# Performance work log

Measured on AMD Instinct MI355X. Metric: run time of the kernel, lower is better.

The kernel has to match this reference:

```python
import jax, jax.numpy as jnp
import numpy as np

# dims
N_USER = 30000; N_ITEM = 30000; HID = 256; HEADS = 4; DH = HID // HEADS
L = 2; E_BUYS = 200000
IMG_D = 512; TASTE_D = 768; NUTR_D = 20; LR = 64; IMG_RANK = 64
EPS = 1e-5
# node type order: 0=user 1=item 2=taste 3=intention 4=image
# edge type order: taste->item, intention->item, image->item, user->item (buys), item->user (bought_by)


def _bn(x, g, b):
    # nn.BatchNorm1d in training mode (biased variance), deterministic
    mu = jnp.mean(x, axis=0)
    var = jnp.mean((x - mu) ** 2, axis=0)
    return (x - mu) * jax.lax.rsqrt(var + EPS) * g + b


def _segment_softmax(logits, seg, n):
    m = jax.ops.segment_max(logits, seg, num_segments=n)
    m = jnp.where(jnp.isfinite(m), m, 0.0)
    e = jnp.exp(logits - m[seg])
    s = jax.ops.segment_sum(e, seg, num_segments=n)
    return e / (s[seg] + 1e-16)


def _model(p, user_id, item_id, buys_src, buys_dst):
    # --- encoders (dropout = identity in eval) ---
    xu = jax.nn.relu(_bn(p['user_emb'][user_id] @ p['user_W'] + p['user_b'], p['user_bn_g'], p['user_bn_b']))
    xi = jax.nn.relu(_bn(p['item_emb'][item_id] @ p['item_W'] + p['item_b'], p['item_bn_g'], p['item_bn_b']))
    ximg = (p['image_feat'] @ p['img_U']) @ p['img_V'] + p['img_b']  # LowRankLinear
    xt = p['taste_feat'] @ p['taste_W'] + p['taste_b']
    xn = p['intent_feat'] @ p['intent_W'] + p['intent_b']
    xs = [xu, xi, xt, xn, ximg]
    assoc = jnp.arange(N_ITEM, dtype=jnp.int32)
    # (src_type, dst_type, src_idx, dst_idx)
    edges = [(2, 1, assoc, assoc), (3, 1, assoc, assoc), (4, 1, assoc, assoc),
             (0, 1, buys_src, buys_dst), (1, 0, buys_dst, buys_src)]
    scale = 1.0 / np.sqrt(DH)
    n_of = [N_USER, N_ITEM]
    for l in range(L):
        k, q, v = [], [], []
        for t in range(5):
            kqv = xs[t] @ p['kqv_W'][l, t] + p['kqv_b'][l, t]
            kk, qq, vv = jnp.split(kqv, 3, axis=1)
            k.append(kk.reshape(-1, HEADS, DH))
            q.append(qq.reshape(-1, HEADS, DH))
            v.append(vv.reshape(-1, HEADS, DH))
        buf = {0: [], 1: []}
        for e, (s, d, si, di) in enumerate(edges):
            # relation-specific per-head transforms of source k/v (all src nodes, then gather)
            ke = jnp.einsum('nhd,hde->nhe', k[s], p['k_rel'][l, e])
            ve = jnp.einsum('nhd,hde->nhe', v[s], p['v_rel'][l, e])
            logit = jnp.sum(q[d][di] * ke[si], axis=-1) * p['p_rel'][l, e] * scale  # [E,H]
            buf[d].append((logit, ve[si], di))
        new_xs = list(xs)
        for d in (0, 1):  # dst node types: user, item
            logits = jnp.concatenate([b[0] for b in buf[d]], axis=0)
            msgs = jnp.concatenate([b[1] for b in buf[d]], axis=0)
            dsts = jnp.concatenate([b[2] for b in buf[d]], axis=0)
            alpha = _segment_softmax(logits, dsts, n_of[d])  # softmax over ALL incoming edges per dst node
            agg = jax.ops.segment_sum(alpha[:, :, None] * msgs, dsts, num_segments=n_of[d])
            o = jax.nn.gelu(agg.reshape(-1, HID), approximate=False) @ p['out_W'][l, d] + p['out_b'][l, d]
            sg = jax.nn.sigmoid(p['skip'][l, d])
            o = sg * o + (1.0 - sg) * xs[d]  # HGTConv learned skip
            o = o + xs[d]                    # MultiModalFusionGAT residual
            o = jax.nn.relu(_bn(o, p['fbn_g'][l, d], p['fbn_b'][l, d]))  # per-type BN+ReLU (dropout eval)
            new_xs[d] = o
        xs = new_xs  # taste/intention/image pass through unchanged
    return jnp.stack(xs, axis=0)  # [5, 30000, HID]


def setup_inputs():
    key = jax.random.key(0)
    ks = iter(jax.random.split(key, 48))
    def nrm(shape, scale=0.05):
        return jax.random.normal(next(ks), shape, dtype=jnp.float32) * scale
    z = lambda *s: jnp.zeros(s, jnp.float32)
    o = lambda *s: jnp.ones(s, jnp.float32)
    inp = {}
    inp['user_id'] = jnp.arange(N_USER, dtype=jnp.int32)
    inp['item_id'] = jnp.arange(N_ITEM, dtype=jnp.int32)
    inp['buys_src'] = jax.random.randint(next(ks), (E_BUYS,), 0, N_USER, dtype=jnp.int32)
    inp['buys_dst'] = jax.random.randint(next(ks), (E_BUYS,), 0, N_ITEM, dtype=jnp.int32)
    inp['image_feat'] = nrm((N_ITEM, IMG_D), 1.0)
    inp['taste_feat'] = nrm((N_ITEM, TASTE_D), 1.0)
    inp['intent_feat'] = nrm((N_ITEM, NUTR_D), 1.0)
    inp['user_emb'] = nrm((N_USER, LR), 0.1)
    inp['user_W'] = nrm((LR, HID)); inp['user_b'] = z(HID)
    inp['user_bn_g'] = o(HID); inp['user_bn_b'] = z(HID)
    inp['item_emb'] = nrm((N_ITEM, LR), 0.1)
    inp['item_W'] = nrm((LR, HID)); inp['item_b'] = z(HID)
    inp['item_bn_g'] = o(HID); inp['item_bn_b'] = z(HID)
    inp['img_U'] = nrm((IMG_D, IMG_RANK)); inp['img_V'] = nrm((IMG_RANK, HID)); inp['img_b'] = z(HID)
    inp['taste_W'] = nrm((TASTE_D, HID)); inp['taste_b'] = z(HID)
    inp['intent_W'] = nrm((NUTR_D, HID)); inp['intent_b'] = z(HID)
    inp['kqv_W'] = nrm((L, 5, HID, 3 * HID)); inp['kqv_b'] = z(L, 5, 3 * HID)
    inp['out_W'] = nrm((L, 5, HID, HID)); inp['out_b'] = z(L, 5, HID)
    inp['k_rel'] = nrm((L, 5, HEADS, DH, DH))
    inp['v_rel'] = nrm((L, 5, HEADS, DH, DH))
    inp['p_rel'] = o(L, 5, HEADS)
    inp['skip'] = o(L, 5)
    inp['fbn_g'] = o(L, 2, HID); inp['fbn_b'] = z(L, 2, HID)
    return inp


def reference(user_id, item_id, buys_src, buys_dst, image_feat, taste_feat, intent_feat,
              user_emb, user_W, user_b, user_bn_g, user_bn_b,
              item_emb, item_W, item_b, item_bn_g, item_bn_b,
              img_U, img_V, img_b, taste_W, taste_b, intent_W, intent_b,
              kqv_W, kqv_b, out_W, out_b, k_rel, v_rel, p_rel, skip, fbn_g, fbn_b):
    p = dict(image_feat=image_feat, taste_feat=taste_feat, intent_feat=intent_feat,
             user_emb=user_emb, user_W=user_W, user_b=user_b, user_bn_g=user_bn_g, user_bn_b=user_bn_b,
             item_emb=item_emb, item_W=item_W, item_b=item_b, item_bn_g=item_bn_g, item_bn_b=item_bn_b,
             img_U=img_U, img_V=img_V, img_b=img_b, taste_W=taste_W, taste_b=taste_b,
             intent_W=intent_W, intent_b=intent_b, kqv_W=kqv_W, kqv_b=kqv_b, out_W=out_W, out_b=out_b,
             k_rel=k_rel, v_rel=v_rel, p_rel=p_rel, skip=skip, fbn_g=fbn_g, fbn_b=fbn_b)
    return _model(p, user_id, item_id, buys_src, buys_dst)
```

## Files before the change

### kernel.cpp

```cpp
#include <hip/hip_runtime.h>
#include <math.h>

#define HID 256
#define EBUY 200000
#define NNODE 30000
#define MP 30080
static const size_t S  = (size_t)NNODE * HID;
static const size_t SP = (size_t)MP * HID;

typedef __attribute__((ext_vector_type(8))) short  short8;
typedef __attribute__((ext_vector_type(4))) float  f32x4;

#define OFF_TASTE 0
#define OFF_INT   196608
#define OFF_IMGU  204800
#define OFF_IMGV  237568
#define OFF_USER  253952
#define OFF_ITEM  270336
#define OFF_OUTW  286720
#define WENC_TOT  548864

__device__ __forceinline__ float gelu_f(float x) {
    return 0.5f * x * (1.0f + erff(x * 0.70710678118654752f));
}
__device__ __forceinline__ unsigned short f2bf(float f) {
    unsigned u = __float_as_uint(f);
    u = (u + 0x7FFFu + ((u >> 16) & 1u)) >> 16;
    return (unsigned short)u;
}
__device__ __forceinline__ float b2f(unsigned short us) {
    return __uint_as_float((unsigned)us << 16);
}
__device__ __forceinline__ void gl_lds16(const unsigned short* g, unsigned short* l) {
    __builtin_amdgcn_global_load_lds(
        (const __attribute__((address_space(1))) unsigned int*)g,
        (__attribute__((address_space(3))) unsigned int*)l, 16, 0, 0);
}

__global__ void conv_pad(const float* __restrict__ in, unsigned short* __restrict__ o,
                         int M, int K, int Kpad)
{
    int i = blockIdx.x * 256 + threadIdx.x;
    if (i >= M * Kpad) return;
    int r = i / Kpad, k = i % Kpad;
    o[i] = (k < K) ? f2bf(in[(size_t)r * K + k]) : (unsigned short)0;
}

__global__ void wtconv_all(const float* __restrict__ taste_W, const float* __restrict__ intent_W,
                           const float* __restrict__ img_U, const float* __restrict__ img_V,
                           const float* __restrict__ user_W, const float* __restrict__ item_W,
                           const float* __restrict__ out_W, unsigned short* __restrict__ WENC)
{
    int i = blockIdx.x * 256 + threadIdx.x;
    if (i >= WENC_TOT) return;
    const float* W; int K, N, Kpad, idx;
    if (i < OFF_INT)        { W = taste_W;  K = 768; N = 256; Kpad = 768; idx = i - OFF_TASTE; }
    else if (i < OFF_IMGU)  { W = intent_W; K = 20;  N = 256; Kpad = 32;  idx = i - OFF_INT; }
    else if (i < OFF_IMGV)  { W = img_U;    K = 512; N = 64;  Kpad = 512; idx = i - OFF_IMGU; }
    else if (i < OFF_USER)  { W = img_V;    K = 64;  N = 256; Kpad = 64;  idx = i - OFF_IMGV; }
    else if (i < OFF_ITEM)  { W = user_W;   K = 64;  N = 256; Kpad = 64;  idx = i - OFF_USER; }
    else if (i < OFF_OUTW)  { W = item_W;   K = 64;  N = 256; Kpad = 64;  idx = i - OFF_ITEM; }
    else {
        int k = (i - OFF_OUTW) >> 16;
        int l = k >> 1, d = k & 1;
        W = out_W + (size_t)(l * 5 + d) * 65536;
        K = 256; N = 256; Kpad = 256; idx = (i - OFF_OUTW) & 65535;
    }
    int n = idx / Kpad, kk = idx % Kpad;
    WENC[i] = (kk < K) ? f2bf(W[(size_t)kk * N + n]) : (unsigned short)0;
}

__global__ void build_kqv(const float* __restrict__ kqv_W, const float* __restrict__ kqv_b,
                          const float* __restrict__ k_rel, const float* __restrict__ v_rel,
                          unsigned short* __restrict__ WKV, float* __restrict__ bKV,
                          unsigned short* __restrict__ WQ, float* __restrict__ bQ)
{
    int s = blockIdx.y;
    int l = s / 5, t = s % 5;
    static const int es[5] = {3, 4, 0, 1, 2};
    int e = es[t];
    int tid = blockIdx.x * 256 + threadIdx.x;
    if (tid >= 257 * 768) return;
    int r = tid / 768, c = tid % 768;
    int cb = c >> 8, cc = c & 255;
    int h = cc >> 6, dd = cc & 63;
    const float* W = kqv_W + (size_t)s * 196608;
    const float* bv = kqv_b + (size_t)s * 768;
    const float* Wrow = (r < 256) ? (W + (size_t)r * 768) : bv;
    if (cb == 1) {
        if (t >= 2) return;
        float outv = Wrow[256 + cc];
        if (r < 256) WQ[(size_t)(l * 2 + t) * 65536 + (size_t)cc * 256 + r] = f2bf(outv);
        else         bQ[(l * 2 + t) * 256 + cc] = outv;
        return;
    }
    const float* R = ((cb == 0) ? k_rel : v_rel) + (size_t)(l * 5 + e) * 16384 + (size_t)h * 4096;
    int sb = (cb == 0) ? 0 : 512;
    float sum = 0.f;
    #pragma unroll 8
    for (int d = 0; d < 64; ++d)
        sum += Wrow[sb + h * 64 + d] * R[d * 64 + dd];
    int col = (cb == 0) ? cc : 256 + cc;
    if (r < 256) WKV[(size_t)s * 131072 + (size_t)col * 256 + r] = f2bf(sum);
    else         bKV[s * 512 + col] = sum;
}

template<int AF32, int GATH2, int BSEL, int EPI>
__launch_bounds__(256)
__global__ void gemm_mfma(const void* __restrict__ Ap, const void* __restrict__ Ap2,
                          const int* __restrict__ g1, const int* __restrict__ g2,
                          const unsigned short* __restrict__ BT0, int bStride,
                          const float* __restrict__ bias0, const float* __restrict__ bias1,
                          int biasStride,
                          float* __restrict__ D0, unsigned short* __restrict__ Db,
                          unsigned short* __restrict__ Db2,
                          int M, int N, int K,
                          const float* __restrict__ skipP, const float* __restrict__ resid,
                          float* __restrict__ bns)
{
    __shared__ union {
        unsigned short AB[4][4096];
        unsigned short O[16384];
    } sm;
    const int tid = threadIdx.x;
    const int gx = gridDim.x;
    int bid = blockIdx.y * gx + blockIdx.x;
    {
        int nwg = gx * gridDim.y;
        int q = nwg >> 3, r = nwg & 7;
        int xc = bid & 7, i = bid >> 3;
        int base = (xc < r) ? xc * (q + 1) : r * (q + 1) + (xc - r) * q;
        bid = base + i;
    }
    const int bx = bid % gx, by = bid / gx;
    const int row0 = by * 128, col0 = bx * 128;
    const int wid = tid >> 6, lane = tid & 63;
    const int wr = wid >> 1, wc = wid & 1;
    const int l16 = lane & 15, kg = lane >> 4;
    const int tt = (BSEL || GATH2) ? (by / 235) : 0;

    const unsigned short* BT = BT0 + (size_t)tt * bStride;
    const float* bias = bias0;
    if (GATH2)              bias = tt ? bias1 : bias0;
    else if (BSEL && bias0) bias = bias0 + (size_t)tt * biasStride;

    f32x4 acc[4][4];
    const f32x4 zero = {0.f, 0.f, 0.f, 0.f};
    #pragma unroll
    for (int i = 0; i < 4; ++i)
        #pragma unroll
        for (int j = 0; j < 4; ++j) acc[i][j] = zero;

    const int lrow = lane >> 2, lchk = lane & 3;
    int cB0 = min(col0 + wid * 32 + lrow, N - 1);
    int cB1 = min(col0 + wid * 32 + 16 + lrow, N - 1);
    const unsigned short* Bp0 = BT + (size_t)cB0 * K + lchk * 8;
    const unsigned short* Bp1 = BT + (size_t)cB1 * K + lchk * 8;
    const int ofs0 = wid * 1024;
    const int ofs1 = wid * 1024 + 512;

    const unsigned short* Ap0b = nullptr; const unsigned short* Ap1b = nullptr;
    const float* Af0 = nullptr; const float* Af1 = nullptr;
    const int rA0 = tid >> 2, rA1 = (tid >> 2) + 64;
    const int q0 = tid & 3;
    if (GATH2) {
        int lr0 = row0 + rA0 - tt * MP; if (lr0 >= NNODE) lr0 = NNODE - 1;
        int lr1 = row0 + rA1 - tt * MP; if (lr1 >= NNODE) lr1 = NNODE - 1;
        const int* gA = tt ? g2 : g1;
        const float* Abase = tt ? (const float*)Ap2 : (const float*)Ap;
        Af0 = Abase + (size_t)gA[lr0] * K;
        Af1 = Abase + (size_t)gA[lr1] * K;
    } else if (AF32) {
        Af0 = (const float*)Ap + (size_t)min(row0 + rA0, M - 1) * K;
        Af1 = (const float*)Ap + (size_t)min(row0 + rA1, M - 1) * K;
    } else {
        int rr0 = min(row0 + wid * 32 + lrow, M - 1);
        int rr1 = min(row0 + wid * 32 + 16 + lrow, M - 1);
        Ap0b = (const unsigned short*)Ap + (size_t)rr0 * K + lchk * 8;
        Ap1b = (const unsigned short*)Ap + (size_t)rr1 * K + lchk * 8;
    }

    const int nt = K >> 5;
    int cur = 0;

    #define STAGE_F32(c, k0) do { \
        float4 x0 = *(const float4*)&Af0[(k0) + q0 * 8]; \
        float4 x1 = *(const float4*)&Af0[(k0) + q0 * 8 + 4]; \
        float4 y0 = *(const float4*)&Af1[(k0) + q0 * 8]; \
        float4 y1 = *(const float4*)&Af1[(k0) + q0 * 8 + 4]; \
        ushort4 u0 = {f2bf(x0.x), f2bf(x0.y), f2bf(x0.z), f2bf(x0.w)}; \
        ushort4 u1 = {f2bf(x1.x), f2bf(x1.y), f2bf(x1.z), f2bf(x1.w)}; \
        ushort4 w0 = {f2bf(y0.x), f2bf(y0.y), f2bf(y0.z), f2bf(y0.w)}; \
        ushort4 w1 = {f2bf(y1.x), f2bf(y1.y), f2bf(y1.z), f2bf(y1.w)}; \
        *(ushort4*)&sm.AB[c][rA0 * 32 + q0 * 8]     = u0; \
        *(ushort4*)&sm.AB[c][rA0 * 32 + q0 * 8 + 4] = u1; \
        *(ushort4*)&sm.AB[c][rA1 * 32 + q0 * 8]     = w0; \
        *(ushort4*)&sm.AB[c][rA1 * 32 + q0 * 8 + 4] = w1; \
        gl_lds16(Bp0 + (k0), &sm.AB[2 + (c)][ofs0]); \
        gl_lds16(Bp1 + (k0), &sm.AB[2 + (c)][ofs1]); \
    } while (0)

    #define STAGE_A(c, k0) do { \
        gl_lds16(Ap0b + (k0), &sm.AB[c][ofs0]); \
        gl_lds16(Ap1b + (k0), &sm.AB[c][ofs1]); \
        gl_lds16(Bp0 + (k0), &sm.AB[2 + (c)][ofs0]); \
        gl_lds16(Bp1 + (k0), &sm.AB[2 + (c)][ofs1]); \
    } while (0)

    #define LOADFRAG(c) do { \
        _Pragma("unroll") \
        for (int i = 0; i < 4; ++i) { \
            af[i]  = *(const short8*)&sm.AB[c][(wr * 64 + i * 16 + l16) * 32 + kg * 8]; \
            bfr[i] = *(const short8*)&sm.AB[2 + (c)][(wc * 64 + i * 16 + l16) * 32 + kg * 8]; \
        } \
    } while (0)

    #define MMAS() do { \
        _Pragma("unroll") \
        for (int i = 0; i < 4; ++i) \
            _Pragma("unroll") \
            for (int j = 0; j < 4; ++j) \
                acc[i][j] = __builtin_amdgcn_mfma_f32_16x16x32_bf16(af[i], bfr[j], acc[i][j], 0, 0, 0); \
    } while (0)

    if (AF32 || GATH2) {
        STAGE_F32(0, 0);
        __syncthreads();
        for (int s = 0; s < nt; ++s) {
            if (s + 1 < nt) STAGE_F32(cur ^ 1, (s + 1) * 32);
            short8 af[4], bfr[4];
            LOADFRAG(cur);
            MMAS();
            __syncthreads();
            cur ^= 1;
        }
    } else {
        STAGE_A(0, 0);
        for (int s = 0; s < nt; ++s) {
            if (s + 1 < nt) {
                STAGE_A(cur ^ 1, (s + 1) * 32);
                asm volatile("s_waitcnt vmcnt(4)" ::: "memory");
            } else {
                asm volatile("s_waitcnt vmcnt(0)" ::: "memory");
            }
            __builtin_amdgcn_s_barrier();
            asm volatile("" ::: "memory");
            short8 af[4], bfr[4];
            LOADFRAG(cur);
            __builtin_amdgcn_s_setprio(1);
            MMAS();
            __builtin_amdgcn_s_setprio(0);
            __builtin_amdgcn_s_barrier();
            asm volatile("" ::: "memory");
            cur ^= 1;
        }
    }
    #undef STAGE_F32
    #undef STAGE_A
    #undef LOADFRAG
    #undef MMAS

    float sg = 0.f;
    if (EPI == 2) sg = 1.f / (1.f + __expf(-skipP[0]));
    #pragma unroll
    for (int j = 0; j < 4; ++j) {
        int lc = wc * 64 + j * 16 + l16;
        int cc = col0 + lc;
        float cs = 0.f, cs2 = 0.f;
        float bv = (bias && cc < N) ? bias[cc] : 0.f;
        #pragma unroll
        for (int i = 0; i < 4; ++i) {
            #pragma unroll
            for (int r = 0; r < 4; ++r) {
                int lr = wr * 64 + i * 16 + kg * 4 + r;
                int rr = row0 + lr;
                float v = acc[i][j][r] + bv;
                if (EPI == 0) {
                    if (D0 && cc < N && rr < M) D0[(size_t)rr * N + cc] = v;
                    sm.O[lr * 128 + ((((lc >> 3) ^ (lr & 7)) << 3) | (lc & 7))] = f2bf(v);
                } else if (EPI == 4 || EPI == 5) {
                    sm.O[lr * 128 + ((((lc >> 3) ^ (lr & 7)) << 3) | (lc & 7))] = f2bf(v);
                } else if (EPI == 6) {
                    D0[(size_t)rr * 256 + cc] = v;
                } else if (EPI == 2) {
                    if (rr < M) {
                        float xo = resid[(size_t)rr * 256 + cc];
                        float o = sg * v + (2.f - sg) * xo;
                        D0[(size_t)rr * 256 + cc] = o;
                        cs += o; cs2 += o * o;
                    }
                }
            }
        }
        if (EPI == 2) {
            cs  += __shfl_xor(cs, 16);  cs  += __shfl_xor(cs, 32);
            cs2 += __shfl_xor(cs2, 16); cs2 += __shfl_xor(cs2, 32);
            if (kg == 0 && cc < N) {
                atomicAdd(&bns[cc], cs);
                atomicAdd(&bns[256 + cc], cs2);
            }
        }
    }
    if (EPI == 0 || EPI == 4 || EPI == 5) {
        __syncthreads();
        unsigned short* T; int ldN, cofs;
        if (EPI == 4)      { T = (col0 < 256) ? Db : Db2; ldN = 256; cofs = col0 & 255; }
        else if (EPI == 5) { T = Db; ldN = 256; cofs = col0; }
        else               { T = Db; ldN = N;   cofs = col0; }
        int nloc = N - col0; if (nloc > 128) nloc = 128;
        if (nloc >= 128) {
            int lr = tid >> 1, half = tid & 1;
            int rr = row0 + lr;
            if (EPI != 0 || rr < M) {
                uint4* dst = (uint4*)&T[(size_t)rr * ldN + cofs + half * 64];
                #pragma unroll
                for (int c = 0; c < 8; ++c) {
                    int ch = half * 8 + c;
                    dst[c] = *(const uint4*)&sm.O[lr * 128 + ((ch ^ (lr & 7)) << 3)];
                }
            }
        } else {
            if (tid < 128) {
                int lr = tid, rr = row0 + lr;
                if (rr < M) {
                    uint4* dst = (uint4*)&T[(size_t)rr * ldN + cofs];
                    #pragma unroll
                    for (int c = 0; c < 8; ++c)
                        dst[c] = *(const uint4*)&sm.O[lr * 128 + ((c ^ (lr & 7)) << 3)];
                }
            }
        }
    }
}

__global__ void edge_hist2(const int* __restrict__ dstk, const int* __restrict__ srck,
                           int* __restrict__ cnt)
{
    int j = blockIdx.x * 256 + threadIdx.x;
    if (j < EBUY) atomicAdd(&cnt[dstk[j]], 1);
    else if (j < 2 * EBUY) atomicAdd(&cnt[NNODE + srck[j - EBUY]], 1);
}

#define SCAN_NB 30
#define SCAN_CH 1000
__global__ void scan_part(const int* __restrict__ cnt, int* __restrict__ bt)
{
    int set = blockIdx.y;
    const int* c = cnt + set * NNODE;
    int b = blockIdx.x;
    int i = b * SCAN_CH + threadIdx.x;
    int v = (threadIdx.x < SCAN_CH && i < NNODE) ? c[i] : 0;
    __shared__ int wsum[16];
    int lane = threadIdx.x & 63, wv = threadIdx.x >> 6;
    for (int o = 32; o; o >>= 1) v += __shfl_down(v, o);
    if (lane == 0) wsum[wv] = v;
    __syncthreads();
    if (threadIdx.x == 0) {
        int s = 0;
        for (int w = 0; w < 16; ++w) s += wsum[w];
        bt[set * 32 + b] = s;
    }
}

__global__ void scan_mid(int* __restrict__ bt, int* __restrict__ off_i, int* __restrict__ off_u)
{
    int set = threadIdx.x;
    if (set >= 2) return;
    int* b = bt + set * 32;
    int s = 0;
    for (int i = 0; i < SCAN_NB; ++i) { int c = b[i]; b[i] = s; s += c; }
    (set ? off_u : off_i)[NNODE] = s;
}

__global__ void scan_final(const int* __restrict__ cnt, const int* __restrict__ bt,
                           int* __restrict__ off_i, int* __restrict__ off_u,
                           int* __restrict__ cur_i, int* __restrict__ cur_u)
{
    int set = blockIdx.y;
    const int* c = cnt + set * NNODE;
    int* off = set ? off_u : off_i;
    int* cur = set ? cur_u : cur_i;
    int b = blockIdx.x;
    int i = b * SCAN_CH + threadIdx.x;
    int v = (threadIdx.x < SCAN_CH && i < NNODE) ? c[i] : 0;
    int lane = threadIdx.x & 63, wv = threadIdx.x >> 6;
    int x = v;
    for (int o = 1; o < 64; o <<= 1) { int t = __shfl_up(x, o); if (lane >= o) x += t; }
    __shared__ int wtot[16];
    if (lane == 63) wtot[wv] = x;
    __syncthreads();
    if (wv == 0) {
        int y = (lane < 16) ? wtot[lane] : 0;
        for (int o = 1; o < 16; o <<= 1) { int t = __shfl_up(y, o); if (lane >= o) y += t; }
        if (lane < 16) wtot[lane] = y;
    }
    __syncthreads();
    int wbase = (wv == 0) ? 0 : wtot[wv - 1];
    int excl = bt[set * 32 + b] + wbase + x - v;
    if (threadIdx.x < SCAN_CH && i < NNODE) { off[i] = excl; cur[i] = excl; }
}

__global__ void edge_place2(const int* __restrict__ dstk, const int* __restrict__ srck,
                            int* __restrict__ cur_i, int* __restrict__ cur_u,
                            int* __restrict__ src_i, int* __restrict__ src_u)
{
    int j = blockIdx.x * 256 + threadIdx.x;
    if (j < EBUY) {
        int pos = atomicAdd(&cur_i[dstk[j]], 1);
        src_i[pos] = srck[j];
    } else if (j < 2 * EBUY) {
        int j2 = j - EBUY;
        int pos = atomicAdd(&cur_u[srck[j2]], 1);
        src_u[pos] = dstk[j2];
    }
}

template<int HAS_ASSOC>
__launch_bounds__(256)
__global__ void attn_gather(const unsigned short* __restrict__ Qd,
                            const unsigned short* __restrict__ KEs,
                            const unsigned short* __restrict__ VEs,
                            const unsigned short* __restrict__ KEa,
                            const unsigned short* __restrict__ VEa,
                            const int* __restrict__ roff, const int* __restrict__ srcArr,
                            const float* __restrict__ pR,
                            unsigned short* __restrict__ AGGb)
{
    int wid = (blockIdx.x * 256 + threadIdx.x) >> 6;
    int lane = threadIdx.x & 63;
    if (wid >= NNODE) return;
    int h = lane >> 4;

    ushort4 qb = *(const ushort4*)(Qd + (size_t)wid * 256 + lane * 4);
    float4 q = {b2f(qb.x), b2f(qb.y), b2f(qb.z), b2f(qb.w)};
    float m = -INFINITY, s = 0.f;
    float4 acc = {0.f, 0.f, 0.f, 0.f};

    if (HAS_ASSOC) {
        #pragma unroll
        for (int e = 0; e < 3; ++e) {
            ushort4 kb = *(const ushort4*)(KEa + (size_t)e * SP + (size_t)wid * 256 + lane * 4);
            float d = q.x * b2f(kb.x) + q.y * b2f(kb.y) + q.z * b2f(kb.z) + q.w * b2f(kb.w);
            for (int off = 8; off; off >>= 1) d += __shfl_xor(d, off, 16);
            float lg = d * pR[e * 4 + h] * 0.125f;
            ushort4 vv = *(const ushort4*)(VEa + (size_t)e * SP + (size_t)wid * 256 + lane * 4);
            float mn = fmaxf(m, lg);
            float so = __expf(m - mn);
            float ev = __expf(lg - mn);
            s = s * so + ev;
            acc.x = acc.x * so + ev * b2f(vv.x);
            acc.y = acc.y * so + ev * b2f(vv.y);
            acc.z = acc.z * so + ev * b2f(vv.z);
            acc.w = acc.w * so + ev * b2f(vv.w);
            m = mn;
        }
    }

    float pb = pR[(HAS_ASSOC ? 12 : 16) + h] * 0.125f;
    int j0 = roff[wid], j1 = roff[wid + 1];
    ushort4 kb = {0,0,0,0}, vv = {0,0,0,0};
    if (j0 < j1) {
        int src0 = srcArr[j0];
        kb = *(const ushort4*)(KEs + (size_t)src0 * 256 + lane * 4);
        vv = *(const ushort4*)(VEs + (size_t)src0 * 256 + lane * 4);
    }
    for (int j = j0; j < j1; ++j) {
        ushort4 ckb = kb, cvv = vv;
        if (j + 1 < j1) {
            int ns = srcArr[j + 1];
            kb = *(const ushort4*)(KEs + (size_t)ns * 256 + lane * 4);
            vv = *(const ushort4*)(VEs + (size_t)ns * 256 + lane * 4);
        }
        float d = q.x * b2f(ckb.x) + q.y * b2f(ckb.y) + q.z * b2f(ckb.z) + q.w * b2f(ckb.w);
        for (int off = 8; off; off >>= 1) d += __shfl_xor(d, off, 16);
        float lg = d * pb;
        float mn = fmaxf(m, lg);
        float so = __expf(m - mn);
        float ev = __expf(lg - mn);
        s = s * so + ev;
        acc.x = acc.x * so + ev * b2f(cvv.x);
        acc.y = acc.y * so + ev * b2f(cvv.y);
        acc.z = acc.z * so + ev * b2f(cvv.z);
        acc.w = acc.w * so + ev * b2f(cvv.w);
        m = mn;
    }

    float inv = 1.f / (s + 1e-16f);
    ushort4 o4;
    o4.x = f2bf(gelu_f(acc.x * inv));
    o4.y = f2bf(gelu_f(acc.y * inv));
    o4.z = f2bf(gelu_f(acc.z * inv));
    o4.w = f2bf(gelu_f(acc.w * inv));
    *(ushort4*)(AGGb + (size_t)wid * 256 + lane * 4) = o4;
}

#define BNB 512
__global__ void bn_stats2(const float* __restrict__ SCRf, float* __restrict__ part)
{
    int tt = blockIdx.y;
    const float* x = SCRf + (size_t)tt * SP;
    int col = threadIdx.x;
    int b = blockIdx.x;
    float s = 0.f, s2 = 0.f;
    int r = b;
    for (; r + 3 * BNB < NNODE; r += 4 * BNB) {
        float v0 = x[(size_t)r * 256 + col];
        float v1 = x[(size_t)(r + BNB) * 256 + col];
        float v2 = x[(size_t)(r + 2 * BNB) * 256 + col];
        float v3 = x[(size_t)(r + 3 * BNB) * 256 + col];
        s += v0 + v1 + v2 + v3;
        s2 += v0 * v0 + v1 * v1 + v2 * v2 + v3 * v3;
    }
    for (; r < NNODE; r += BNB) {
        float v = x[(size_t)r * 256 + col];
        s += v; s2 += v * v;
    }
    part[((size_t)tt * BNB + b) * 512 + col] = s;
    part[((size_t)tt * BNB + b) * 512 + 256 + col] = s2;
}

__global__ void bn_fin2(const float* __restrict__ part,
                        const float* __restrict__ g0, const float* __restrict__ b0,
                        const float* __restrict__ g1, const float* __restrict__ b1,
                        float* __restrict__ scsh)
{
    int tid = threadIdx.x;
    int tt = tid >> 8, col = tid & 255;
    const float* p = part + (size_t)tt * BNB * 512;
    float s = 0.f, s2 = 0.f;
    #pragma unroll 4
    for (int b = 0; b < BNB; ++b) { s += p[b * 512 + col]; s2 += p[b * 512 + 256 + col]; }
    float mu = s / (float)NNODE;
    float var = s2 / (float)NNODE - mu * mu;
    float sc = rsqrtf(var + 1e-5f) * (tt ? g1 : g0)[col];
    scsh[tt * 512 + col] = sc;
    scsh[tt * 512 + 256 + col] = (tt ? b1 : b0)[col] - mu * sc;
}

__global__ void bn_apply2(const float* __restrict__ SCRf, const float* __restrict__ scsh,
                          float* __restrict__ out, unsigned short* __restrict__ XBall)
{
    const int Q4 = NNODE * 64;
    for (int i = blockIdx.x * 256 + threadIdx.x; i < 2 * Q4; i += gridDim.x * 256) {
        int tt = (i >= Q4) ? 1 : 0;
        int local = i - tt * Q4;
        int c4 = local & 63;
        float4 sc4 = *(const float4*)&scsh[tt * 512 + c4 * 4];
        float4 sh4 = *(const float4*)&scsh[tt * 512 + 256 + c4 * 4];
        float4 v = ((const float4*)(SCRf + (size_t)tt * SP))[local];
        v.x = fmaxf(v.x * sc4.x + sh4.x, 0.f);
        v.y = fmaxf(v.y * sc4.y + sh4.y, 0.f);
        v.z = fmaxf(v.z * sc4.z + sh4.z, 0.f);
        v.w = fmaxf(v.w * sc4.w + sh4.w, 0.f);
        ((float4*)(out + (size_t)tt * S))[local] = v;
        ushort4 u = {f2bf(v.x), f2bf(v.y), f2bf(v.z), f2bf(v.w)};
        ((ushort4*)(XBall + (size_t)tt * SP))[local] = u;
    }
}

__global__ void bn_find(const float* __restrict__ bns, const float* __restrict__ g,
                        const float* __restrict__ b_, float* __restrict__ scsh)
{
    int col = threadIdx.x;
    float s = bns[col], s2 = bns[256 + col];
    float mu = s / (float)NNODE;
    float var = s2 / (float)NNODE - mu * mu;
    float sc = rsqrtf(var + 1e-5f) * g[col];
    scsh[col] = sc;
    scsh[256 + col] = b_[col] - mu * sc;
}

__global__ void bn_apply1(const float* __restrict__ x, const float* __restrict__ scsh,
                          float* __restrict__ y, unsigned short* __restrict__ yb)
{
    const int Q4 = NNODE * 64;
    int c4 = threadIdx.x & 63;
    float4 sc4 = *(const float4*)&scsh[c4 * 4];
    float4 sh4 = *(const float4*)&scsh[256 + c4 * 4];
    for (int i = blockIdx.x * 256 + threadIdx.x; i < Q4; i += gridDim.x * 256) {
        float4 v = ((const float4*)x)[i];
        v.x = fmaxf(v.x * sc4.x + sh4.x, 0.f);
        v.y = fmaxf(v.y * sc4.y + sh4.y, 0.f);
        v.z = fmaxf(v.z * sc4.z + sh4.z, 0.f);
        v.w = fmaxf(v.w * sc4.w + sh4.w, 0.f);
        ((float4*)y)[i] = v;
        ushort4 u = {f2bf(v.x), f2bf(v.y), f2bf(v.z), f2bf(v.w)};
        ((ushort4*)yb)[i] = u;
    }
}

extern "C" void kernel_launch(void* const* d_in, const int* in_sizes, int n_in,
                              void* d_out, int out_size, void* d_ws, size_t ws_size,
                              hipStream_t stream)
{
    const int*   user_id    = (const int*)d_in[0];
    const int*   item_id    = (const int*)d_in[1];
    const int*   buys_src   = (const int*)d_in[2];
    const int*   buys_dst   = (const int*)d_in[3];
    const float* image_feat = (const float*)d_in[4];
    const float* taste_feat = (const float*)d_in[5];
    const float* intent_feat= (const float*)d_in[6];
    const float* user_emb   = (const float*)d_in[7];
    const float* user_W     = (const float*)d_in[8];
    const float* user_b     = (const float*)d_in[9];
    const float* user_bn_g  = (const float*)d_in[10];
    const float* user_bn_b  = (const float*)d_in[11];
    const float* item_emb   = (const float*)d_in[12];
    const float* item_W     = (const float*)d_in[13];
    const float* item_b     = (const float*)d_in[14];
    const float* item_bn_g  = (const float*)d_in[15];
    const float* item_bn_b  = (const float*)d_in[16];
    const float* img_U      = (const float*)d_in[17];
    const float* img_V      = (const float*)d_in[18];
    const float* img_b      = (const float*)d_in[19];
    const float* taste_W    = (const float*)d_in[20];
    const float* taste_b    = (const float*)d_in[21];
    const float* intent_W   = (const float*)d_in[22];
    const float* intent_b   = (const float*)d_in[23];
    const float* kqv_W      = (const float*)d_in[24];
    const float* kqv_b      = (const float*)d_in[25];
    const float* out_W      = (const float*)d_in[26];
    const float* out_b      = (const float*)d_in[27];
    const float* k_rel      = (const float*)d_in[28];
    const float* v_rel      = (const float*)d_in[29];
    const float* p_rel      = (const float*)d_in[30];
    const float* skip       = (const float*)d_in[31];
    const float* fbn_g      = (const float*)d_in[32];
    const float* fbn_b      = (const float*)d_in[33];

    float* out = (float*)d_out;
    float* ws  = (float*)d_ws;

    float* SCRf = ws;
    float* BNSp = SCRf + 2 * SP;
    float* BNS  = BNSp + 2 * BNB * 512;
    float* SCSH = BNS + 512;
    float* bKV  = SCSH + 1024;
    float* bQ   = bKV + 5120;
    unsigned short* QB    = (unsigned short*)(bQ + 1024);
    unsigned short* XBall = QB + 2 * SP;
    unsigned short* KEall = XBall + 5 * SP;
    unsigned short* VEall = KEall + 5 * SP;
    unsigned short* AGB   = VEall + 5 * SP;
    unsigned short* IMB   = AGB + S;
    unsigned short* IPB   = IMB + (size_t)NNODE * 64;
    unsigned short* WKV   = IPB + (size_t)NNODE * 32;
    unsigned short* WQ    = WKV + 1310720;
    unsigned short* WENC  = WQ + 262144;
    int* cnt   = (int*)(WENC + WENC_TOT);
    int* off_i = cnt + 2 * NNODE;
    int* off_u = off_i + NNODE + 1;
    int* cur_i = off_u + NNODE + 1;
    int* cur_u = cur_i + NNODE;
    int* src_i = cur_u + NNODE;
    int* src_u = src_i + EBUY;
    int* bt    = src_u + EBUY;

    size_t need = (size_t)((char*)(bt + 64) - (char*)ws);
    if (ws_size < need) return;

    hipMemsetAsync(cnt, 0, 2 * NNODE * 4, stream);
    edge_hist2<<<(2 * EBUY + 255) / 256, 256, 0, stream>>>(buys_dst, buys_src, cnt);
    scan_part<<<dim3(SCAN_NB, 2), 1024, 0, stream>>>(cnt, bt);
    scan_mid<<<1, 64, 0, stream>>>(bt, off_i, off_u);
    scan_final<<<dim3(SCAN_NB, 2), 1024, 0, stream>>>(cnt, bt, off_i, off_u, cur_i, cur_u);
    edge_place2<<<(2 * EBUY + 255) / 256, 256, 0, stream>>>(buys_dst, buys_src, cur_i, cur_u, src_i, src_u);

    wtconv_all<<<(WENC_TOT + 255) / 256, 256, 0, stream>>>(taste_W, intent_W, img_U, img_V,
                                                           user_W, item_W, out_W, WENC);
    build_kqv<<<dim3(771, 10), 256, 0, stream>>>(kqv_W, kqv_b, k_rel, v_rel, WKV, bKV, WQ, bQ);
    conv_pad<<<(NNODE * 32 + 255) / 256, 256, 0, stream>>>(intent_feat, IPB, NNODE, 20, 32);

    hipLaunchKernelGGL((gemm_mfma<1,0,0,0>), dim3(2,235), dim3(256), 0, stream,
        taste_feat, nullptr, nullptr, nullptr, WENC + OFF_TASTE, 0, taste_b, nullptr, 0,
        out + 2*S, XBall + 2*SP, nullptr, NNODE, 256, 768, nullptr, nullptr, nullptr);
    hipLaunchKernelGGL((gemm_mfma<0,0,0,0>), dim3(2,235), dim3(256), 0, stream,
        IPB, nullptr, nullptr, nullptr, WENC + OFF_INT, 0, intent_b, nullptr, 0,
        out + 3*S, XBall + 3*SP, nullptr, NNODE, 256, 32, nullptr, nullptr, nullptr);
    hipLaunchKernelGGL((gemm_mfma<1,0,0,0>), dim3(1,235), dim3(256), 0, stream,
        image_feat, nullptr, nullptr, nullptr, WENC + OFF_IMGU, 0, nullptr, nullptr, 0,
        nullptr, IMB, nullptr, NNODE, 64, 512, nullptr, nullptr, nullptr);
    hipLaunchKernelGGL((gemm_mfma<0,0,0,0>), dim3(2,235), dim3(256), 0, stream,
        IMB, nullptr, nullptr, nullptr, WENC + OFF_IMGV, 0, img_b, nullptr, 0,
        out + 4*S, XBall + 4*SP, nullptr, NNODE, 256, 64, nullptr, nullptr, nullptr);
    hipLaunchKernelGGL((gemm_mfma<1,1,1,6>), dim3(2,470), dim3(256), 0, stream,
        user_emb, item_emb, user_id, item_id, WENC + OFF_USER, 16384, user_b, item_b, 0,
        SCRf, nullptr, nullptr, 2*MP, 256, 64, nullptr, nullptr, nullptr);
    bn_stats2<<<dim3(BNB, 2), 256, 0, stream>>>(SCRf, BNSp);
    bn_fin2<<<1, 512, 0, stream>>>(BNSp, user_bn_g, user_bn_b, item_bn_g, item_bn_b, SCSH);
    bn_apply2<<<960, 256, 0, stream>>>(SCRf, SCSH, out, XBall);

    for (int l = 0; l < 2; ++l) {
        hipLaunchKernelGGL((gemm_mfma<0,0,1,4>), dim3(4, 5*235), dim3(256), 0, stream,
            XBall, nullptr, nullptr, nullptr, WKV + (size_t)l*5*131072, 131072,
            bKV + l*5*512, nullptr, 512, nullptr, KEall, VEall,
            5*MP, 512, 256, nullptr, nullptr, nullptr);
        hipLaunchKernelGGL((gemm_mfma<0,0,1,5>), dim3(2, 2*235), dim3(256), 0, stream,
            XBall, nullptr, nullptr, nullptr, WQ + (size_t)l*2*65536, 65536,
            bQ + l*2*256, nullptr, 256, nullptr, QB, nullptr,
            2*MP, 256, 256, nullptr, nullptr, nullptr);
        hipLaunchKernelGGL((attn_gather<1>), dim3((NNODE*64 + 255)/256), dim3(256), 0, stream,
            QB + SP, KEall, VEall, KEall + 2*SP, VEall + 2*SP, off_i, src_i,
            p_rel + l*20, AGB);
        hipMemsetAsync(BNS, 0, 512 * 4, stream);
        hipLaunchKernelGGL((gemm_mfma<0,0,0,2>), dim3(2,235), dim3(256), 0, stream,
            AGB, nullptr, nullptr, nullptr, WENC + OFF_OUTW + (size_t)(l*2+1)*65536, 0,
            out_b + (l*5+1)*256, nullptr, 0, SCRf, nullptr, nullptr,
            NNODE, 256, 256, skip + (l*5+1), out + S, BNS);
        bn_find<<<1, 256, 0, stream>>>(BNS, fbn_g + (l*2+1)*256, fbn_b + (l*2+1)*256, SCSH);
        bn_apply1<<<960, 256, 0, stream>>>(SCRf, SCSH, out + S, XBall + SP);
        hipLaunchKernelGGL((attn_gather<0>), dim3((NNODE*64 + 255)/256), dim3(256), 0, stream,
            QB, KEall + SP, VEall + SP, nullptr, nullptr, off_u, src_u,
            p_rel + l*20, AGB);
        hipMemsetAsync(BNS, 0, 512 * 4, stream);
        hipLaunchKernelGGL((gemm_mfma<0,0,0,2>), dim3(2,235), dim3(256), 0, stream,
            AGB, nullptr, nullptr, nullptr, WENC + OFF_OUTW + (size_t)(l*2+0)*65536, 0,
            out_b + (l*5+0)*256, nullptr, 0, SCRf, nullptr, nullptr,
            NNODE, 256, 256, skip + (l*5+0), out, BNS);
        bn_find<<<1, 256, 0, stream>>>(BNS, fbn_g + (l*2+0)*256, fbn_b + (l*2+0)*256, SCSH);
        bn_apply1<<<960, 256, 0, stream>>>(SCRf, SCSH, out, XBall);
    }
}
```

Measured before the change: 1.039 ms.

## Fuse K/V/Q projection GEMMs into one 256-row-tile kernel with LDS swizzle

```diff
diff --git a/kernel.cpp b/kernel.cpp
--- a/kernel.cpp
+++ b/kernel.cpp
@@ -4,9 +4,9 @@
 #define HID 256
 #define EBUY 200000
 #define NNODE 30000
-#define MP 30080
+#define MPD 30208
 static const size_t S  = (size_t)NNODE * HID;
-static const size_t SP = (size_t)MP * HID;
+static const size_t SP = (size_t)MPD * HID;
 
 typedef __attribute__((ext_vector_type(8))) short  short8;
 typedef __attribute__((ext_vector_type(4))) float  f32x4;
@@ -35,6 +35,12 @@
     __builtin_amdgcn_global_load_lds(
         (const __attribute__((address_space(1))) unsigned int*)g,
         (__attribute__((address_space(3))) unsigned int*)l, 16, 0, 0);
+}
+__device__ __forceinline__ int xcd_swz(int bid, int nwg) {
+    int q = nwg >> 3, r = nwg & 7;
+    int xc = bid & 7, i = bid >> 3;
+    int base = (xc < r) ? xc * (q + 1) : r * (q + 1) + (xc - r) * q;
+    return base + i;
 }
 
 __global__ void conv_pad(const float* __restrict__ in, unsigned short* __restrict__ o,
@@ -72,8 +78,7 @@
 
 __global__ void build_kqv(const float* __restrict__ kqv_W, const float* __restrict__ kqv_b,
                           const float* __restrict__ k_rel, const float* __restrict__ v_rel,
-                          unsigned short* __restrict__ WKV, float* __restrict__ bKV,
-                          unsigned short* __restrict__ WQ, float* __restrict__ bQ)
+                          unsigned short* __restrict__ WALL, float* __restrict__ bALL)
 {
     int s = blockIdx.y;
     int l = s / 5, t = s % 5;
@@ -90,8 +95,8 @@
     if (cb == 1) {
         if (t >= 2) return;
         float outv = Wrow[256 + cc];
-        if (r < 256) WQ[(size_t)(l * 2 + t) * 65536 + (size_t)cc * 256 + r] = f2bf(outv);
-        else         bQ[(l * 2 + t) * 256 + cc] = outv;
+        if (r < 256) WALL[(size_t)s * 196608 + (size_t)(512 + cc) * 256 + r] = f2bf(outv);
+        else         bALL[s * 768 + 512 + cc] = outv;
         return;
     }
     const float* R = ((cb == 0) ? k_rel : v_rel) + (size_t)(l * 5 + e) * 16384 + (size_t)h * 4096;
@@ -101,19 +106,17 @@
     for (int d = 0; d < 64; ++d)
         sum += Wrow[sb + h * 64 + d] * R[d * 64 + dd];
     int col = (cb == 0) ? cc : 256 + cc;
-    if (r < 256) WKV[(size_t)s * 131072 + (size_t)col * 256 + r] = f2bf(sum);
-    else         bKV[s * 512 + col] = sum;
-}
-
-template<int AF32, int GATH2, int BSEL, int EPI>
+    if (r < 256) WALL[(size_t)s * 196608 + (size_t)col * 256 + r] = f2bf(sum);
+    else         bALL[s * 768 + col] = sum;
+}
+
+template<int AF32, int GATH2, int EPI>
 __launch_bounds__(256)
 __global__ void gemm_mfma(const void* __restrict__ Ap, const void* __restrict__ Ap2,
                           const int* __restrict__ g1, const int* __restrict__ g2,
-                          const unsigned short* __restrict__ BT0, int bStride,
+                          const unsigned short* __restrict__ BT0,
                           const float* __restrict__ bias0, const float* __restrict__ bias1,
-                          int biasStride,
                           float* __restrict__ D0, unsigned short* __restrict__ Db,
-                          unsigned short* __restrict__ Db2,
                           int M, int N, int K,
                           const float* __restrict__ skipP, const float* __restrict__ resid,
                           float* __restrict__ bns)
@@ -124,25 +127,18 @@
     } sm;
     const int tid = threadIdx.x;
     const int gx = gridDim.x;
-    int bid = blockIdx.y * gx + blockIdx.x;
-    {
-        int nwg = gx * gridDim.y;
-        int q = nwg >> 3, r = nwg & 7;
-        int xc = bid & 7, i = bid >> 3;
-        int base = (xc < r) ? xc * (q + 1) : r * (q + 1) + (xc - r) * q;
-        bid = base + i;
-    }
+    int bid = xcd_swz(blockIdx.y * gx + blockIdx.x, gx * gridDim.y);
     const int bx = bid % gx, by = bid / gx;
     const int row0 = by * 128, col0 = bx * 128;
     const int wid = tid >> 6, lane = tid & 63;
     const int wr = wid >> 1, wc = wid & 1;
     const int l16 = lane & 15, kg = lane >> 4;
-    const int tt = (BSEL || GATH2) ? (by / 235) : 0;
-
-    const unsigned short* BT = BT0 + (size_t)tt * bStride;
+    const int tt = GATH2 ? (by / 236) : 0;
+
+    const unsigned short* BT = BT0;
     const float* bias = bias0;
-    if (GATH2)              bias = tt ? bias1 : bias0;
-    else if (BSEL && bias0) bias = bias0 + (size_t)tt * biasStride;
+    if (GATH2) bias = tt ? bias1 : bias0;
+    if (GATH2 && tt) BT = BT0 + 16384;
 
     f32x4 acc[4][4];
     const f32x4 zero = {0.f, 0.f, 0.f, 0.f};
@@ -152,10 +148,11 @@
         for (int j = 0; j < 4; ++j) acc[i][j] = zero;
 
     const int lrow = lane >> 2, lchk = lane & 3;
+    const int gsw = (lchk ^ ((lrow >> 1) & 3)) * 8;
     int cB0 = min(col0 + wid * 32 + lrow, N - 1);
     int cB1 = min(col0 + wid * 32 + 16 + lrow, N - 1);
-    const unsigned short* Bp0 = BT + (size_t)cB0 * K + lchk * 8;
-    const unsigned short* Bp1 = BT + (size_t)cB1 * K + lchk * 8;
+    const unsigned short* Bp0 = BT + (size_t)cB0 * K + gsw;
+    const unsigned short* Bp1 = BT + (size_t)cB1 * K + gsw;
     const int ofs0 = wid * 1024;
     const int ofs1 = wid * 1024 + 512;
 
@@ -163,9 +160,10 @@
     const float* Af0 = nullptr; const float* Af1 = nullptr;
     const int rA0 = tid >> 2, rA1 = (tid >> 2) + 64;
     const int q0 = tid & 3;
+    const int wsw = (q0 ^ ((rA0 >> 1) & 3)) * 8;
     if (GATH2) {
-        int lr0 = row0 + rA0 - tt * MP; if (lr0 >= NNODE) lr0 = NNODE - 1;
-        int lr1 = row0 + rA1 - tt * MP; if (lr1 >= NNODE) lr1 = NNODE - 1;
+        int lr0 = row0 + rA0 - tt * MPD; if (lr0 >= NNODE) lr0 = NNODE - 1;
+        int lr1 = row0 + rA1 - tt * MPD; if (lr1 >= NNODE) lr1 = NNODE - 1;
         const int* gA = tt ? g2 : g1;
         const float* Abase = tt ? (const float*)Ap2 : (const float*)Ap;
         Af0 = Abase + (size_t)gA[lr0] * K;
@@ -176,12 +174,13 @@
     } else {
         int rr0 = min(row0 + wid * 32 + lrow, M - 1);
         int rr1 = min(row0 + wid * 32 + 16 + lrow, M - 1);
-        Ap0b = (const unsigned short*)Ap + (size_t)rr0 * K + lchk * 8;
-        Ap1b = (const unsigned short*)Ap + (size_t)rr1 * K + lchk * 8;
+        Ap0b = (const unsigned short*)Ap + (size_t)rr0 * K + gsw;
+        Ap1b = (const unsigned short*)Ap + (size_t)rr1 * K + gsw;
     }
 
     const int nt = K >> 5;
     int cur = 0;
+    const int rsw = ((l16 >> 1) & 3);
 
     #define STAGE_F32(c, k0) do { \
         float4 x0 = *(const float4*)&Af0[(k0) + q0 * 8]; \
@@ -192,10 +191,10 @@
         ushort4 u1 = {f2bf(x1.x), f2bf(x1.y), f2bf(x1.z), f2bf(x1.w)}; \
         ushort4 w0 = {f2bf(y0.x), f2bf(y0.y), f2bf(y0.z), f2bf(y0.w)}; \
         ushort4 w1 = {f2bf(y1.x), f2bf(y1.y), f2bf(y1.z), f2bf(y1.w)}; \
-        *(ushort4*)&sm.AB[c][rA0 * 32 + q0 * 8]     = u0; \
-        *(ushort4*)&sm.AB[c][rA0 * 32 + q0 * 8 + 4] = u1; \
-        *(ushort4*)&sm.AB[c][rA1 * 32 + q0 * 8]     = w0; \
-        *(ushort4*)&sm.AB[c][rA1 * 32 + q0 * 8 + 4] = w1; \
+        *(ushort4*)&sm.AB[c][rA0 * 32 + wsw]     = u0; \
+        *(ushort4*)&sm.AB[c][rA0 * 32 + wsw + 4] = u1; \
+        *(ushort4*)&sm.AB[c][rA1 * 32 + wsw]     = w0; \
+        *(ushort4*)&sm.AB[c][rA1 * 32 + wsw + 4] = w1; \
         gl_lds16(Bp0 + (k0), &sm.AB[2 + (c)][ofs0]); \
         gl_lds16(Bp1 + (k0), &sm.AB[2 + (c)][ofs1]); \
     } while (0)
@@ -210,8 +209,8 @@
     #define LOADFRAG(c) do { \
         _Pragma("unroll") \
         for (int i = 0; i < 4; ++i) { \
-            af[i]  = *(const short8*)&sm.AB[c][(wr * 64 + i * 16 + l16) * 32 + kg * 8]; \
-            bfr[i] = *(const short8*)&sm.AB[2 + (c)][(wc * 64 + i * 16 + l16) * 32 + kg * 8]; \
+            af[i]  = *(const short8*)&sm.AB[c][(wr * 64 + i * 16 + l16) * 32 + (kg ^ rsw) * 8]; \
+            bfr[i] = *(const short8*)&sm.AB[2 + (c)][(wc * 64 + i * 16 + l16) * 32 + (kg ^ rsw) * 8]; \
         } \
     } while (0)
 
@@ -278,8 +277,6 @@
                 if (EPI == 0) {
                     if (D0 && cc < N && rr < M) D0[(size_t)rr * N + cc] = v;
                     sm.O[lr * 128 + ((((lc >> 3) ^ (lr & 7)) << 3) | (lc & 7))] = f2bf(v);
-                } else if (EPI == 4 || EPI == 5) {
-                    sm.O[lr * 128 + ((((lc >> 3) ^ (lr & 7)) << 3) | (lc & 7))] = f2bf(v);
                 } else if (EPI == 6) {
                     D0[(size_t)rr * 256 + cc] = v;
                 } else if (EPI == 2) {
@@ -301,18 +298,14 @@
             }
         }
     }
-    if (EPI == 0 || EPI == 4 || EPI == 5) {
+    if (EPI == 0) {
         __syncthreads();
-        unsigned short* T; int ldN, cofs;
-        if (EPI == 4)      { T = (col0 < 256) ? Db : Db2; ldN = 256; cofs = col0 & 255; }
-        else if (EPI == 5) { T = Db; ldN = 256; cofs = col0; }
-        else               { T = Db; ldN = N;   cofs = col0; }
         int nloc = N - col0; if (nloc > 128) nloc = 128;
         if (nloc >= 128) {
             int lr = tid >> 1, half = tid & 1;
             int rr = row0 + lr;
-            if (EPI != 0 || rr < M) {
-                uint4* dst = (uint4*)&T[(size_t)rr * ldN + cofs + half * 64];
+            if (rr < M) {
+                uint4* dst = (uint4*)&Db[(size_t)rr * N + col0 + half * 64];
                 #pragma unroll
                 for (int c = 0; c < 8; ++c) {
                     int ch = half * 8 + c;
@@ -323,13 +316,132 @@
             if (tid < 128) {
                 int lr = tid, rr = row0 + lr;
                 if (rr < M) {
-                    uint4* dst = (uint4*)&T[(size_t)rr * ldN + cofs];
+                    uint4* dst = (uint4*)&Db[(size_t)rr * N + col0];
                     #pragma unroll
                     for (int c = 0; c < 8; ++c)
                         dst[c] = *(const uint4*)&sm.O[lr * 128 + ((c ^ (lr & 7)) << 3)];
                 }
             }
         }
+    }
+}
+
+__launch_bounds__(256)
+__global__ void gemm_kvq(const unsigned short* __restrict__ A,
+                         const unsigned short* __restrict__ BT0,
+                         const float* __restrict__ bias0,
+                         unsigned short* __restrict__ KE, unsigned short* __restrict__ VE,
+                         unsigned short* __restrict__ QB)
+{
+    __shared__ union {
+        struct { unsigned short A[2][8192]; unsigned short B[2][4096]; } s;
+        unsigned short O[16384];
+    } sm;
+    const int tid = threadIdx.x;
+    int bid = xcd_swz(blockIdx.y * 6 + blockIdx.x, 6 * gridDim.y);
+    const int bx = bid % 6, by = bid / 6;
+    const int tt = by / 118;
+    if (tt >= 2 && bx >= 4) return;
+    const int row0 = by * 256, col0 = bx * 128;
+    const int wid = tid >> 6, lane = tid & 63;
+    const int l16 = lane & 15, kg = lane >> 4;
+    const unsigned short* BT = BT0 + (size_t)tt * 196608;
+    const float* bias = bias0 + tt * 768;
+
+    f32x4 acc[4][8];
+    const f32x4 zero = {0.f, 0.f, 0.f, 0.f};
+    #pragma unroll
+    for (int i = 0; i < 4; ++i)
+        #pragma unroll
+        for (int j = 0; j < 8; ++j) acc[i][j] = zero;
+
+    const int lrow = lane >> 2, lchk = lane & 3;
+    const int gsw = (lchk ^ ((lrow >> 1) & 3)) * 8;
+    const unsigned short* ApL[4];
+    #pragma unroll
+    for (int q = 0; q < 4; ++q)
+        ApL[q] = A + (size_t)(row0 + wid * 64 + q * 16 + lrow) * 256 + gsw;
+    const unsigned short* BpL[2];
+    #pragma unroll
+    for (int q = 0; q < 2; ++q)
+        BpL[q] = BT + (size_t)(col0 + wid * 32 + q * 16 + lrow) * 256 + gsw;
+
+    const int aofs = wid * 2048;
+    const int bofs = wid * 1024;
+
+    #define STAGE(c, k0) do { \
+        _Pragma("unroll") \
+        for (int q = 0; q < 4; ++q) gl_lds16(ApL[q] + (k0), &sm.s.A[c][aofs + q * 512]); \
+        _Pragma("unroll") \
+        for (int q = 0; q < 2; ++q) gl_lds16(BpL[q] + (k0), &sm.s.B[c][bofs + q * 512]); \
+    } while (0)
+
+    const int rsw = ((l16 >> 1) & 3);
+    int cur = 0;
+    STAGE(0, 0);
+    for (int s = 0; s < 8; ++s) {
+        if (s + 1 < 8) {
+            STAGE(cur ^ 1, (s + 1) * 32);
+            asm volatile("s_waitcnt vmcnt(6)" ::: "memory");
+        } else {
+            asm volatile("s_waitcnt vmcnt(0)" ::: "memory");
+        }
+        __builtin_amdgcn_s_barrier();
+        asm volatile("" ::: "memory");
+        short8 af[4], bfr[8];
+        #pragma unroll
+        for (int i = 0; i < 4; ++i)
+            af[i] = *(const short8*)&sm.s.A[cur][(wid * 64 + i * 16 + l16) * 32 + (kg ^ rsw) * 8];
+        #pragma unroll
+        for (int j = 0; j < 8; ++j)
+            bfr[j] = *(const short8*)&sm.s.B[cur][(j * 16 + l16) * 32 + (kg ^ rsw) * 8];
+        __builtin_amdgcn_s_setprio(1);
+        #pragma unroll
+        for (int i = 0; i < 4; ++i)
+            #pragma unroll
+            for (int j = 0; j < 8; ++j)
+                acc[i][j] = __builtin_amdgcn_mfma_f32_16x16x32_bf16(af[i], bfr[j], acc[i][j], 0, 0, 0);
+        __builtin_amdgcn_s_setprio(0);
+        __builtin_amdgcn_s_barrier();
+        asm volatile("" ::: "memory");
+        cur ^= 1;
+    }
+    #undef STAGE
+
+    int dsel = bx >> 1;
+    unsigned short* T = (dsel == 0) ? KE : ((dsel == 1) ? VE : QB);
+    const int cofs0 = (bx & 1) * 128;
+    #pragma unroll
+    for (int p = 0; p < 2; ++p) {
+        if ((wid >> 1) == p) {
+            int rb = (wid & 1) * 64;
+            #pragma unroll
+            for (int j = 0; j < 8; ++j) {
+                int lc = j * 16 + l16;
+                float bv = bias[col0 + lc];
+                #pragma unroll
+                for (int i = 0; i < 4; ++i) {
+                    #pragma unroll
+                    for (int r = 0; r < 4; ++r) {
+                        int olr = rb + i * 16 + kg * 4 + r;
+                        float v = acc[i][j][r] + bv;
+                        sm.O[olr * 128 + ((((lc >> 3) ^ (olr & 7)) << 3) | (lc & 7))] = f2bf(v);
+                    }
+                }
+            }
+        }
+        __syncthreads();
+        {
+            int lr = tid >> 1, half = tid & 1;
+            int rr = row0 + p * 128 + lr;
+            uint4* dst = (uint4*)&T[(size_t)rr * 256 + cofs0 + half * 64];
+            #pragma unroll
+            for (int c = 0; c < 8; ++c) {
+                int ch = half * 8 + c;
+                dst[c] = *(const uint4*)&sm.O[lr * 128 + ((ch ^ (lr & 7)) << 3)];
+            }
+        }
+        __syncthreads();
     }
 }
 
@@ -635,18 +747,16 @@
     float* BNSp = SCRf + 2 * SP;
     float* BNS  = BNSp + 2 * BNB * 512;
     float* SCSH = BNS + 512;
-    float* bKV  = SCSH + 1024;
-    float* bQ   = bKV + 5120;
-    unsigned short* QB    = (unsigned short*)(bQ + 1024);
+    float* bALL = SCSH + 1024;
+    unsigned short* QB    = (unsigned short*)(bALL + 7680);
     unsigned short* XBall = QB + 2 * SP;
     unsigned short* KEall = XBall + 5 * SP;
     unsigned short* VEall = KEall + 5 * SP;
     unsigned short* AGB   = VEall + 5 * SP;
     unsigned short* IMB   = AGB + S;
     unsigned short* IPB   = IMB + (size_t)NNODE * 64;
-    unsigned short* WKV   = IPB + (size_t)NNODE * 32;
-    unsigned short* WQ    = WKV + 1310720;
-    unsigned short* WENC  = WQ + 262144;
+    unsigned short* WALL  = IPB + (size_t)NNODE * 32;
+    unsigned short* WENC  = WALL + (size_t)10 * 196608;
     int* cnt   = (int*)(WENC + WENC_TOT);
     int* off_i = cnt + 2 * NNODE;
     int* off_u = off_i + NNODE + 1;
@@ -668,44 +778,38 @@
 
     wtconv_all<<<(WENC_TOT + 255) / 256, 256, 0, stream>>>(taste_W, intent_W, img_U, img_V,
                                                            user_W, item_W, out_W, WENC);
-    build_kqv<<<dim3(771, 10), 256, 0, stream>>>(kqv_W, kqv_b, k_rel, v_rel, WKV, bKV, WQ, bQ);
+    build_kqv<<<dim3(771, 10), 256, 0, stream>>>(kqv_W, kqv_b, k_rel, v_rel, WALL, bALL);
     conv_pad<<<(NNODE * 32 + 255) / 256, 256, 0, stream>>>(intent_feat, IPB, NNODE, 20, 32);
 
-    hipLaunchKernelGGL((gemm_mfma<1,0,0,0>), dim3(2,235), dim3(256), 0, stream,
-        taste_feat, nullptr, nullptr, nullptr, WENC + OFF_TASTE, 0, taste_b, nullptr, 0,
-        out + 2*S, XBall + 2*SP, nullptr, NNODE, 256, 768, nullptr, nullptr, nullptr);
-    hipLaunchKernelGGL((gemm_mfma<0,0,0,0>), dim3(2,235), dim3(256), 0, stream,
-        IPB, nullptr, nullptr, nullptr, WENC + OFF_INT, 0, intent_b, nullptr, 0,
-        out + 3*S, XBall + 3*SP, nullptr, NNODE, 256, 32, nullptr, nullptr, nullptr);
-    hipLaunchKernelGGL((gemm_mfma<1,0,0,0>), dim3(1,235), dim3(256), 0, stream,
-        image_feat, nullptr, nullptr, nullptr, WENC + OFF_IMGU, 0, nullptr, nullptr, 0,
-        nullptr, IMB, nullptr, NNODE, 64, 512, nullptr, nullptr, nullptr);
-    hipLaunchKernelGGL((gemm_mfma<0,0,0,0>), dim3(2,235), dim3(256), 0, stream,
-        IMB, nullptr, nullptr, nullptr, WENC + OFF_IMGV, 0, img_b, nullptr, 0,
-        out + 4*S, XBall + 4*SP, nullptr, NNODE, 256, 64, nullptr, nullptr, nullptr);
-    hipLaunchKernelGGL((gemm_mfma<1,1,1,6>), dim3(2,470), dim3(256), 0, stream,
-        user_emb, item_emb, user_id, item_id, WENC + OFF_USER, 16384, user_b, item_b, 0,
-        SCRf, nullptr, nullptr, 2*MP, 256, 64, nullptr, nullptr, nullptr);
+    hipLaunchKernelGGL((gemm_mfma<1,0,0>), dim3(2,235), dim3(256), 0, stream,
+        taste_feat, nullptr, nullptr, nullptr, WENC + OFF_TASTE, taste_b, nullptr,
+        out + 2*S, XBall + 2*SP, NNODE, 256, 768, nullptr, nullptr, nullptr);
+    hipLaunchKernelGGL((gemm_mfma<0,0,0>), dim3(2,235), dim3(256), 0, stream,
+        IPB, nullptr, nullptr, nullptr, WENC + OFF_INT, intent_b, nullptr,
+        out + 3*S, XBall + 3*SP, NNODE, 256, 32, nullptr, nullptr, nullptr);
+    hipLaunchKernelGGL((gemm_mfma<1,0,0>), dim3(1,235), dim3(256), 0, stream,
+        image_feat, nullptr, nullptr, nullptr, WENC + OFF_IMGU, nullptr, nullptr,
+        nullptr, IMB, NNODE, 64, 512, nullptr, nullptr, nullptr);
+    hipLaunchKernelGGL((gemm_mfma<0,0,0>), dim3(2,235), dim3(256), 0, stream,
+        IMB, nullptr, nullptr, nullptr, WENC + OFF_IMGV, img_b, nullptr,
+        out + 4*S, XBall + 4*SP, NNODE, 256, 64, nullptr, nullptr, nullptr);
+    hipLaunchKernelGGL((gemm_mfma<1,1,6>), dim3(2,472), dim3(256), 0, stream,
+        user_emb, item_emb, user_id, item_id, WENC + OFF_USER, user_b, item_b,
+        SCRf, nullptr, 2*MPD, 256, 64, nullptr, nullptr, nullptr);
     bn_stats2<<<dim3(BNB, 2), 256, 0, stream>>>(SCRf, BNSp);
     bn_fin2<<<1, 512, 0, stream>>>(BNSp, user_bn_g, user_bn_b, item_bn_g, item_bn_b, SCSH);
     bn_apply2<<<960, 256, 0, stream>>>(SCRf, SCSH, out, XBall);
 
     for (int l = 0; l < 2; ++l) {
-        hipLaunchKernelGGL((gemm_mfma<0,0,1,4>), dim3(4, 5*235), dim3(256), 0, stream,
-            XBall, nullptr, nullptr, nullptr, WKV + (size_t)l*5*131072, 131072,
-            bKV + l*5*512, nullptr, 512, nullptr, KEall, VEall,
-            5*MP, 512, 256, nullptr, nullptr, nullptr);
-        hipLaunchKernelGGL((gemm_mfma<0,0,1,5>), dim3(2, 2*235), dim3(256), 0, stream,
-            XBall, nullptr, nullptr, nullptr, WQ + (size_t)l*2*65536, 65536,
-            bQ + l*2*256, nullptr, 256, nullptr, QB, nullptr,
-            2*MP, 256, 256, nullptr, nullptr, nullptr);
+        hipLaunchKernelGGL(gemm_kvq, dim3(6, 5*118), dim3(256), 0, stream,
+            XBall, WALL + (size_t)l*5*196608, bALL + l*5*768, KEall, VEall, QB);
         hipLaunchKernelGGL((attn_gather<1>), dim3((NNODE*64 + 255)/256), dim3(256), 0, stream,
             QB + SP, KEall, VEall, KEall + 2*SP, VEall + 2*SP, off_i, src_i,
             p_rel + l*20, AGB);
         hipMemsetAsync(BNS, 0, 512 * 4, stream);
-        hipLaunchKernelGGL((gemm_mfma<0,0,0,2>), dim3(2,235), dim3(256), 0, stream,
-            AGB, nullptr, nullptr, nullptr, WENC + OFF_OUTW + (size_t)(l*2+1)*65536, 0,
-            out_b + (l*5+1)*256, nullptr, 0, SCRf, nullptr, nullptr,
+        hipLaunchKernelGGL((gemm_mfma<0,0,2>), dim3(2,235), dim3(256), 0, stream,
+            AGB, nullptr, nullptr, nullptr, WENC + OFF_OUTW + (size_t)(l*2+1)*65536,
+            out_b + (l*5+1)*256, nullptr, SCRf, nullptr,
             NNODE, 256, 256, skip + (l*5+1), out + S, BNS);
         bn_find<<<1, 256, 0, stream>>>(BNS, fbn_g + (l*2+1)*256, fbn_b + (l*2+1)*256, SCSH);
         bn_apply1<<<960, 256, 0, stream>>>(SCRf, SCSH, out + S, XBall + SP);
@@ -713,9 +817,9 @@
             QB, KEall + SP, VEall + SP, nullptr, nullptr, off_u, src_u,
             p_rel + l*20, AGB);
         hipMemsetAsync(BNS, 0, 512 * 4, stream);
-        hipLaunchKernelGGL((gemm_mfma<0,0,0,2>), dim3(2,235), dim3(256), 0, stream,
-            AGB, nullptr, nullptr, nullptr, WENC + OFF_OUTW + (size_t)(l*2+0)*65536, 0,
-            out_b + (l*5+0)*256, nullptr, 0, SCRf, nullptr, nullptr,
+        hipLaunchKernelGGL((gemm_mfma<0,0,2>), dim3(2,235), dim3(256), 0, stream,
+            AGB, nullptr, nullptr, nullptr, WENC + OFF_OUTW + (size_t)(l*2+0)*65536,
+            out_b + (l*5+0)*256, nullptr, SCRf, nullptr,
             NNODE, 256, 256, skip + (l*5+0), out, BNS);
         bn_find<<<1, 256, 0, stream>>>(BNS, fbn_g + (l*2+0)*256, fbn_b + (l*2+0)*256, SCSH);
         bn_apply1<<<960, 256, 0, stream>>>(SCRf, SCSH, out, XBall);
```

Measured after the change: 1.146 ms. +10.3%, slower.
